# Kernel optimization log

Measured on AMD Instinct MI355X. Metric: run time of the kernel, lower is better.

## Reference

```python
import jax, jax.numpy as jnp
import numpy as np

T, B, I, H = 512, 256, 256, 512  # seq_len, batch, input_size, hidden_size


def setup_inputs() -> dict:
    key = jax.random.key(0)
    ks = jax.random.split(key, 7)
    sc = 1.0 / np.sqrt(H)  # PyTorch nn.RNN init scale ~ U(-1/sqrt(H), 1/sqrt(H)); use scaled normal
    return {
        "x": jax.random.normal(ks[0], (T, B, I), dtype=jnp.float32),
        "w_ih": jax.random.normal(ks[1], (H, I), dtype=jnp.float32) * sc,
        "w_hh": jax.random.normal(ks[2], (H, H), dtype=jnp.float32) * sc,
        "b_ih": jax.random.normal(ks[3], (H,), dtype=jnp.float32) * sc,
        "b_hh": jax.random.normal(ks[4], (H,), dtype=jnp.float32) * sc,
        "w_fc": jax.random.normal(ks[5], (I, H), dtype=jnp.float32) * sc,
        "b_fc": jax.random.normal(ks[6], (I,), dtype=jnp.float32) * sc,
    }


def reference(x, w_ih, w_hh, b_ih, b_hh, w_fc, b_fc):
    # Single-layer tanh RNN (h0 = 0): h_t = tanh(x_t W_ih^T + b_ih + h_{t-1} W_hh^T + b_hh)
    # Hoist the input projection out of the recurrence (one big GEMM).
    xp = jnp.einsum('tbi,hi->tbh', x, w_ih) + b_ih + b_hh  # [T,B,H]
    h0 = jnp.zeros((x.shape[1], w_hh.shape[0]), dtype=x.dtype)

    def step(h, xt):
        h_new = jnp.tanh(xt + h @ w_hh.T)
        return h_new, h_new

    _, hs = jax.lax.scan(step, h0, xp)  # hs: [T,B,H]
    # Output head: Linear(hidden_size -> input_size)
    return jnp.einsum('tbh,oh->tbo', hs, w_fc) + b_fc  # [T,B,I]
```

## Files before the change

### kernel.cpp

```cpp
#include <hip/hip_runtime.h>
#include <hip/hip_bf16.h>

#define T_ 512
#define B_ 256
#define I_ 256
#define H_ 512

#define NG 16
#define NS 4

#define RING_WPG (H_ * 8)
#define RING_BYTES (2ull * NG * RING_WPG * 8)

typedef _Float16 f16x8 __attribute__((ext_vector_type(8)));
typedef float f32x4 __attribute__((ext_vector_type(4)));

__device__ __forceinline__ float tanh_fast(float v) {
  float e = __expf(2.0f * v);
  return 1.0f - 2.0f / (e + 1.0f);
}

__device__ __forceinline__ f16x8 cvt8(const float4 a, const float4 b) {
  f16x8 f;
  f[0] = (_Float16)a.x; f[1] = (_Float16)a.y; f[2] = (_Float16)a.z; f[3] = (_Float16)a.w;
  f[4] = (_Float16)b.x; f[5] = (_Float16)b.y; f[6] = (_Float16)b.z; f[7] = (_Float16)b.w;
  return f;
}

__device__ __forceinline__ unsigned long long pack2h(_Float16 a, _Float16 b, unsigned tag) {
  unsigned ua = __builtin_bit_cast(unsigned short, a);
  unsigned ub = __builtin_bit_cast(unsigned short, b);
  return (unsigned long long)(ua | (ub << 16)) | ((unsigned long long)tag << 32);
}

__global__ __launch_bounds__(256, 1) void rnn_recurrence(
    const float* __restrict__ x,
    const float* __restrict__ w_ih,
    const float* __restrict__ w_hh,
    const float* __restrict__ b_ih,
    const float* __restrict__ b_hh,
    unsigned long long* __restrict__ ring,
    _Float16* __restrict__ hs)
{
  const int tid  = threadIdx.x;
  const int lane = tid & 63;
  const int w    = tid >> 6;
  const int bid  = blockIdx.x;
  const int g    = bid & 15;
  const int s    = bid >> 4;
  const int r0   = g * 16;
  const int c0   = s * 128;
  const int lrow = lane & 15;
  const int quad = lane >> 4;
  const int kq   = quad * 8;

  __shared__ _Float16 hbuf[16][512 + 8];
  __shared__ _Float16 xbuf[16][256 + 8];

  f16x8 whh0[16], whh1[16];
  f16x8 wih0[8], wih1[8];
  const int n0c = c0 + (2 * w + 0) * 16 + lrow;
  const int n1c = c0 + (2 * w + 1) * 16 + lrow;
  const float bias0 = b_ih[n0c] + b_hh[n0c];
  const float bias1 = b_ih[n1c] + b_hh[n1c];
  #pragma unroll
  for (int kt = 0; kt < 16; ++kt) {
    const int k = kt * 32 + kq;
    whh0[kt] = cvt8(*(const float4*)(w_hh + (size_t)n0c * H_ + k),
                    *(const float4*)(w_hh + (size_t)n0c * H_ + k + 4));
    whh1[kt] = cvt8(*(const float4*)(w_hh + (size_t)n1c * H_ + k),
                    *(const float4*)(w_hh + (size_t)n1c * H_ + k + 4));
  }
  #pragma unroll
  for (int kt = 0; kt < 8; ++kt) {
    const int k = kt * 32 + kq;
    wih0[kt] = cvt8(*(const float4*)(w_ih + (size_t)n0c * I_ + k),
                    *(const float4*)(w_ih + (size_t)n0c * I_ + k + 4));
    wih1[kt] = cvt8(*(const float4*)(w_ih + (size_t)n1c * I_ + k),
                    *(const float4*)(w_ih + (size_t)n1c * I_ + k + 4));
  }

  int colf[12], prow[12];
  int roff[12];
  #pragma unroll
  for (int j = 0; j < 12; ++j) {
    const int wdx = tid + j * 256;
    const int rs  = wdx >> 10;
    const int sl  = rs + (rs >= s ? 1 : 0);
    const int c   = (wdx >> 3) & 127;
    const int p   = wdx & 7;
    colf[j] = sl * 128 + c;
    prow[j] = p * 2;
    roff[j] = colf[j] * 8 + p;
  }

  {
    const int row = tid >> 4, ch = tid & 15;
    f16x8 z = {0, 0, 0, 0, 0, 0, 0, 0};
    *(f16x8*)(&hbuf[row][c0 + ch * 8]) = z;
  }

  for (int t = 0; t < T_; ++t) {
    {
      const float* src = x + ((size_t)t * B_ + r0) * I_;
      #pragma unroll
      for (int c = tid; c < 512; c += 256) {
        const int row = c >> 5;
        const int col = (c & 31) * 8;
        *(f16x8*)(&xbuf[row][col]) =
            cvt8(*(const float4*)(src + (size_t)row * I_ + col),
                 *(const float4*)(src + (size_t)row * I_ + col + 4));
      }
    }
    {
      const unsigned long long* rg =
          ring + ((size_t)((t & 1) ? NG : 0) + g) * RING_WPG;
      unsigned long long v[12];
      #pragma unroll
      for (int j = 0; j < 12; ++j)
        v[j] = __hip_atomic_load(&rg[roff[j]], __ATOMIC_RELAXED,
                                 __HIP_MEMORY_SCOPE_AGENT);
      bool again = true;
      while (again) {
        again = false;
        #pragma unroll
        for (int j = 0; j < 12; ++j) {
          if ((unsigned)(v[j] >> 32) != (unsigned)t) {
            v[j] = __hip_atomic_load(&rg[roff[j]], __ATOMIC_RELAXED,
                                     __HIP_MEMORY_SCOPE_AGENT);
            again = true;
          }
        }
      }
      #pragma unroll
      for (int j = 0; j < 12; ++j) {
        const unsigned lo = (unsigned)v[j];
        hbuf[prow[j] + 0][colf[j]] =
            __builtin_bit_cast(_Float16, (unsigned short)(lo & 0xffff));
        hbuf[prow[j] + 1][colf[j]] =
            __builtin_bit_cast(_Float16, (unsigned short)(lo >> 16));
      }
    }
    __syncthreads();

    if (t > 0) {
      const int row = tid >> 4, ch = tid & 15;
      *(uint4*)(hs + ((size_t)(t - 1) * B_ + r0 + row) * H_ + c0 + ch * 8) =
          *(const uint4*)(&hbuf[row][c0 + ch * 8]);
    }

    f32x4 a0a = {0.f,0.f,0.f,0.f}, a0b = {0.f,0.f,0.f,0.f};
    f32x4 a1a = {0.f,0.f,0.f,0.f}, a1b = {0.f,0.f,0.f,0.f};
    #pragma unroll
    for (int kt = 0; kt < 8; ++kt) {
      const f16x8 a = *(const f16x8*)(&hbuf[lrow][kt * 32 + kq]);
      a0a = __builtin_amdgcn_mfma_f32_16x16x32_f16(a, whh0[kt], a0a, 0, 0, 0);
      a1a = __builtin_amdgcn_mfma_f32_16x16x32_f16(a, whh1[kt], a1a, 0, 0, 0);
    }
    #pragma unroll
    for (int kt = 8; kt < 16; ++kt) {
      const f16x8 a = *(const f16x8*)(&hbuf[lrow][kt * 32 + kq]);
      a0b = __builtin_amdgcn_mfma_f32_16x16x32_f16(a, whh0[kt], a0b, 0, 0, 0);
      a1b = __builtin_amdgcn_mfma_f32_16x16x32_f16(a, whh1[kt], a1b, 0, 0, 0);
    }
    #pragma unroll
    for (int kt = 0; kt < 4; ++kt) {
      const f16x8 a = *(const f16x8*)(&xbuf[lrow][kt * 32 + kq]);
      a0a = __builtin_amdgcn_mfma_f32_16x16x32_f16(a, wih0[kt], a0a, 0, 0, 0);
      a1a = __builtin_amdgcn_mfma_f32_16x16x32_f16(a, wih1[kt], a1a, 0, 0, 0);
    }
    #pragma unroll
    for (int kt = 4; kt < 8; ++kt) {
      const f16x8 a = *(const f16x8*)(&xbuf[lrow][kt * 32 + kq]);
      a0b = __builtin_amdgcn_mfma_f32_16x16x32_f16(a, wih0[kt], a0b, 0, 0, 0);
      a1b = __builtin_amdgcn_mfma_f32_16x16x32_f16(a, wih1[kt], a1b, 0, 0, 0);
    }
    const f32x4 acc0 = a0a + a0b;
    const f32x4 acc1 = a1a + a1b;

    __syncthreads();

    _Float16 e0[4], e1[4];
    #pragma unroll
    for (int r = 0; r < 4; ++r) {
      e0[r] = (_Float16)tanh_fast(acc0[r] + bias0);
      e1[r] = (_Float16)tanh_fast(acc1[r] + bias1);
      hbuf[quad * 4 + r][n0c] = e0[r];
      hbuf[quad * 4 + r][n1c] = e1[r];
    }
    {
      unsigned long long* rn =
          ring + ((size_t)(((t + 1) & 1) ? NG : 0) + g) * RING_WPG;
      const unsigned tag = (unsigned)(t + 1);
      __hip_atomic_store(&rn[n0c * 8 + quad * 2 + 0], pack2h(e0[0], e0[1], tag),
                         __ATOMIC_RELAXED, __HIP_MEMORY_SCOPE_AGENT);
      __hip_atomic_store(&rn[n0c * 8 + quad * 2 + 1], pack2h(e0[2], e0[3], tag),
                         __ATOMIC_RELAXED, __HIP_MEMORY_SCOPE_AGENT);
      __hip_atomic_store(&rn[n1c * 8 + quad * 2 + 0], pack2h(e1[0], e1[1], tag),
                         __ATOMIC_RELAXED, __HIP_MEMORY_SCOPE_AGENT);
      __hip_atomic_store(&rn[n1c * 8 + quad * 2 + 1], pack2h(e1[2], e1[3], tag),
                         __ATOMIC_RELAXED, __HIP_MEMORY_SCOPE_AGENT);
    }
  }

  __syncthreads();
  {
    const int row = tid >> 4, ch = tid & 15;
    *(uint4*)(hs + ((size_t)(T_ - 1) * B_ + r0 + row) * H_ + c0 + ch * 8) =
        *(const uint4*)(&hbuf[row][c0 + ch * 8]);
  }
}

__global__ __launch_bounds__(256) void fc_head(
    const _Float16* __restrict__ hs,
    const float* __restrict__ w_fc,
    const float* __restrict__ b_fc,
    float* __restrict__ out)
{
  const int tid  = threadIdx.x;
  const int lane = tid & 63;
  const int w    = tid >> 6;
  const int wm   = w & 1;
  const int wn   = w >> 1;
  const int m0   = blockIdx.x * 64;
  const int n0   = blockIdx.y * 64;
  const int lrow = lane & 15;
  const int quad = lane >> 4;
  const int kq   = quad * 8;

  __shared__ _Float16 As[64][32 + 8];
  __shared__ _Float16 Bs[64][32 + 8];

  f32x4 acc00 = {0.f,0.f,0.f,0.f}, acc01 = {0.f,0.f,0.f,0.f};
  f32x4 acc10 = {0.f,0.f,0.f,0.f}, acc11 = {0.f,0.f,0.f,0.f};

  const int srow = tid >> 2;
  const int skc  = (tid & 3) * 8;

  for (int k0 = 0; k0 < H_; k0 += 32) {
    *(uint4*)(&As[srow][skc]) =
        *(const uint4*)(hs + (size_t)(m0 + srow) * H_ + k0 + skc);
    *(f16x8*)(&Bs[srow][skc]) =
        cvt8(*(const float4*)(w_fc + (size_t)(n0 + srow) * H_ + k0 + skc),
             *(const float4*)(w_fc + (size_t)(n0 + srow) * H_ + k0 + skc + 4));
    __syncthreads();

    const f16x8 a0 = *(const f16x8*)(&As[wm * 32 + lrow][kq]);
    const f16x8 a1 = *(const f16x8*)(&As[wm * 32 + 16 + lrow][kq]);
    const f16x8 b0 = *(const f16x8*)(&Bs[wn * 32 + lrow][kq]);
    const f16x8 b1 = *(const f16x8*)(&Bs[wn * 32 + 16 + lrow][kq]);
    acc00 = __builtin_amdgcn_mfma_f32_16x16x32_f16(a0, b0, acc00, 0, 0, 0);
    acc01 = __builtin_amdgcn_mfma_f32_16x16x32_f16(a0, b1, acc01, 0, 0, 0);
    acc10 = __builtin_amdgcn_mfma_f32_16x16x32_f16(a1, b0, acc10, 0, 0, 0);
    acc11 = __builtin_amdgcn_mfma_f32_16x16x32_f16(a1, b1, acc11, 0, 0, 0);
    __syncthreads();
  }

  #pragma unroll
  for (int ni = 0; ni < 2; ++ni) {
    const int col = n0 + wn * 32 + ni * 16 + lrow;
    const float bf = b_fc[col];
    #pragma unroll
    for (int mi = 0; mi < 2; ++mi) {
      const f32x4 a = (mi == 0) ? (ni == 0 ? acc00 : acc01)
                                : (ni == 0 ? acc10 : acc11);
      #pragma unroll
      for (int r = 0; r < 4; ++r) {
        const int rowm = m0 + wm * 32 + mi * 16 + quad * 4 + r;
        out[(size_t)rowm * I_ + col] = a[r] + bf;
      }
    }
  }
}

extern "C" void kernel_launch(void* const* d_in, const int* in_sizes, int n_in,
                              void* d_out, int out_size, void* d_ws, size_t ws_size,
                              hipStream_t stream) {
  const float* x    = (const float*)d_in[0];
  const float* w_ih = (const float*)d_in[1];
  const float* w_hh = (const float*)d_in[2];
  const float* b_ih = (const float*)d_in[3];
  const float* b_hh = (const float*)d_in[4];
  const float* w_fc = (const float*)d_in[5];
  const float* b_fc = (const float*)d_in[6];
  float* out = (float*)d_out;

  unsigned long long* ring = (unsigned long long*)d_ws;
  _Float16* hs = (_Float16*)((char*)d_ws + RING_BYTES);

  hipMemsetAsync(d_ws, 0, (size_t)NG * RING_WPG * 8, stream);

  rnn_recurrence<<<64, 256, 0, stream>>>(x, w_ih, w_hh, b_ih, b_hh, ring, hs);
  fc_head<<<dim3(2048, 4), 256, 0, stream>>>(hs, w_fc, b_fc, out);
}
```

Baseline: 1.996 ms.

## Overlap local-slice MFMAs and x loads with remote hidden-state polling

```diff
diff --git a/kernel.cpp b/kernel.cpp
--- a/kernel.cpp
+++ b/kernel.cpp
@@ -65,7 +65,8 @@
   const float bias1 = b_ih[n1c] + b_hh[n1c];
   #pragma unroll
   for (int kt = 0; kt < 16; ++kt) {
-    const int k = kt * 32 + kq;
+    const int pk = (s * 4 + kt) & 15;
+    const int k  = pk * 32 + kq;
     whh0[kt] = cvt8(*(const float4*)(w_hh + (size_t)n0c * H_ + k),
                     *(const float4*)(w_hh + (size_t)n0c * H_ + k + 4));
     whh1[kt] = cvt8(*(const float4*)(w_hh + (size_t)n1c * H_ + k),
@@ -80,7 +81,6 @@
                     *(const float4*)(w_ih + (size_t)n1c * I_ + k + 4));
   }
 
-  int colf[12], prow[12];
   int roff[12];
   #pragma unroll
   for (int j = 0; j < 12; ++j) {
@@ -89,9 +89,7 @@
     const int sl  = rs + (rs >= s ? 1 : 0);
     const int c   = (wdx >> 3) & 127;
     const int p   = wdx & 7;
-    colf[j] = sl * 128 + c;
-    prow[j] = p * 2;
-    roff[j] = colf[j] * 8 + p;
+    roff[j] = (sl * 128 + c) * 8 + p;
   }
 
   {
@@ -99,27 +97,46 @@
     f16x8 z = {0, 0, 0, 0, 0, 0, 0, 0};
     *(f16x8*)(&hbuf[row][c0 + ch * 8]) = z;
   }
+  __syncthreads();
+
+  const int xrow = tid >> 5;
+  const int xcol = (tid & 31) * 8;
 
   for (int t = 0; t < T_; ++t) {
+    const unsigned long long* rg =
+        ring + ((size_t)((t & 1) ? NG : 0) + g) * RING_WPG;
+    unsigned long long v[12];
+    #pragma unroll
+    for (int j = 0; j < 12; ++j)
+      v[j] = __hip_atomic_load(&rg[roff[j]], __ATOMIC_RELAXED,
+                               __HIP_MEMORY_SCOPE_AGENT);
+
+    const float* src = x + ((size_t)t * B_ + r0) * I_;
+    const float4 xv0 = *(const float4*)(src + (size_t)xrow * I_ + xcol);
+    const float4 xv1 = *(const float4*)(src + (size_t)xrow * I_ + xcol + 4);
+    const float4 xv2 = *(const float4*)(src + (size_t)(xrow + 8) * I_ + xcol);
+    const float4 xv3 = *(const float4*)(src + (size_t)(xrow + 8) * I_ + xcol + 4);
+
+    if (t > 0) {
+      const int row = tid >> 4, ch = tid & 15;
+      *(uint4*)(hs + ((size_t)(t - 1) * B_ + r0 + row) * H_ + c0 + ch * 8) =
+          *(const uint4*)(&hbuf[row][c0 + ch * 8]);
+    }
+
+    f32x4 a0a = {0.f,0.f,0.f,0.f}, a0b = {0.f,0.f,0.f,0.f};
+    f32x4 a1a = {0.f,0.f,0.f,0.f}, a1b = {0.f,0.f,0.f,0.f};
+    #pragma unroll
+    for (int kt = 0; kt < 4; ++kt) {
+      const int pk = (s * 4 + kt) & 15;
+      const f16x8 a = *(const f16x8*)(&hbuf[lrow][pk * 32 + kq]);
+      a0b = __builtin_amdgcn_mfma_f32_16x16x32_f16(a, whh0[kt], a0b, 0, 0, 0);
+      a1b = __builtin_amdgcn_mfma_f32_16x16x32_f16(a, whh1[kt], a1b, 0, 0, 0);
+    }
+
+    *(f16x8*)(&xbuf[xrow][xcol])     = cvt8(xv0, xv1);
+    *(f16x8*)(&xbuf[xrow + 8][xcol]) = cvt8(xv2, xv3);
+
     {
-      const float* src = x + ((size_t)t * B_ + r0) * I_;
-      #pragma unroll
-      for (int c = tid; c < 512; c += 256) {
-        const int row = c >> 5;
-        const int col = (c & 31) * 8;
-        *(f16x8*)(&xbuf[row][col]) =
-            cvt8(*(const float4*)(src + (size_t)row * I_ + col),
-                 *(const float4*)(src + (size_t)row * I_ + col + 4));
-      }
-    }
-    {
-      const unsigned long long* rg =
-          ring + ((size_t)((t & 1) ? NG : 0) + g) * RING_WPG;
-      unsigned long long v[12];
-      #pragma unroll
-      for (int j = 0; j < 12; ++j)
-        v[j] = __hip_atomic_load(&rg[roff[j]], __ATOMIC_RELAXED,
-                                 __HIP_MEMORY_SCOPE_AGENT);
       bool again = true;
       while (again) {
         again = false;
@@ -134,59 +151,48 @@
       }
       #pragma unroll
       for (int j = 0; j < 12; ++j) {
+        const int col = roff[j] >> 3;
+        const int pr  = (roff[j] & 7) * 2;
         const unsigned lo = (unsigned)v[j];
-        hbuf[prow[j] + 0][colf[j]] =
+        hbuf[pr + 0][col] =
             __builtin_bit_cast(_Float16, (unsigned short)(lo & 0xffff));
-        hbuf[prow[j] + 1][colf[j]] =
+        hbuf[pr + 1][col] =
             __builtin_bit_cast(_Float16, (unsigned short)(lo >> 16));
       }
     }
     __syncthreads();
 
-    if (t > 0) {
-      const int row = tid >> 4, ch = tid & 15;
-      *(uint4*)(hs + ((size_t)(t - 1) * B_ + r0 + row) * H_ + c0 + ch * 8) =
-          *(const uint4*)(&hbuf[row][c0 + ch * 8]);
-    }
-
-    f32x4 a0a = {0.f,0.f,0.f,0.f}, a0b = {0.f,0.f,0.f,0.f};
-    f32x4 a1a = {0.f,0.f,0.f,0.f}, a1b = {0.f,0.f,0.f,0.f};
+    #pragma unroll
+    for (int kt = 4; kt < 16; ++kt) {
+      const int pk = (s * 4 + kt) & 15;
+      const f16x8 a = *(const f16x8*)(&hbuf[lrow][pk * 32 + kq]);
+      if (kt < 10) {
+        a0a = __builtin_amdgcn_mfma_f32_16x16x32_f16(a, whh0[kt], a0a, 0, 0, 0);
+        a1a = __builtin_amdgcn_mfma_f32_16x16x32_f16(a, whh1[kt], a1a, 0, 0, 0);
+      } else {
+        a0b = __builtin_amdgcn_mfma_f32_16x16x32_f16(a, whh0[kt], a0b, 0, 0, 0);
+        a1b = __builtin_amdgcn_mfma_f32_16x16x32_f16(a, whh1[kt], a1b, 0, 0, 0);
+      }
+    }
     #pragma unroll
     for (int kt = 0; kt < 8; ++kt) {
-      const f16x8 a = *(const f16x8*)(&hbuf[lrow][kt * 32 + kq]);
-      a0a = __builtin_amdgcn_mfma_f32_16x16x32_f16(a, whh0[kt], a0a, 0, 0, 0);
-      a1a = __builtin_amdgcn_mfma_f32_16x16x32_f16(a, whh1[kt], a1a, 0, 0, 0);
-    }
-    #pragma unroll
-    for (int kt = 8; kt < 16; ++kt) {
-      const f16x8 a = *(const f16x8*)(&hbuf[lrow][kt * 32 + kq]);
-      a0b = __builtin_amdgcn_mfma_f32_16x16x32_f16(a, whh0[kt], a0b, 0, 0, 0);
-      a1b = __builtin_amdgcn_mfma_f32_16x16x32_f16(a, whh1[kt], a1b, 0, 0, 0);
-    }
-    #pragma unroll
-    for (int kt = 0; kt < 4; ++kt) {
       const f16x8 a = *(const f16x8*)(&xbuf[lrow][kt * 32 + kq]);
-      a0a = __builtin_amdgcn_mfma_f32_16x16x32_f16(a, wih0[kt], a0a, 0, 0, 0);
-      a1a = __builtin_amdgcn_mfma_f32_16x16x32_f16(a, wih1[kt], a1a, 0, 0, 0);
-    }
-    #pragma unroll
-    for (int kt = 4; kt < 8; ++kt) {
-      const f16x8 a = *(const f16x8*)(&xbuf[lrow][kt * 32 + kq]);
-      a0b = __builtin_amdgcn_mfma_f32_16x16x32_f16(a, wih0[kt], a0b, 0, 0, 0);
-      a1b = __builtin_amdgcn_mfma_f32_16x16x32_f16(a, wih1[kt], a1b, 0, 0, 0);
+      if (kt < 4) {
+        a0a = __builtin_amdgcn_mfma_f32_16x16x32_f16(a, wih0[kt], a0a, 0, 0, 0);
+        a1a = __builtin_amdgcn_mfma_f32_16x16x32_f16(a, wih1[kt], a1a, 0, 0, 0);
+      } else {
+        a0b = __builtin_amdgcn_mfma_f32_16x16x32_f16(a, wih0[kt], a0b, 0, 0, 0);
+        a1b = __builtin_amdgcn_mfma_f32_16x16x32_f16(a, wih1[kt], a1b, 0, 0, 0);
+      }
     }
     const f32x4 acc0 = a0a + a0b;
     const f32x4 acc1 = a1a + a1b;
-
-    __syncthreads();
 
     _Float16 e0[4], e1[4];
     #pragma unroll
     for (int r = 0; r < 4; ++r) {
       e0[r] = (_Float16)tanh_fast(acc0[r] + bias0);
       e1[r] = (_Float16)tanh_fast(acc1[r] + bias1);
-      hbuf[quad * 4 + r][n0c] = e0[r];
-      hbuf[quad * 4 + r][n1c] = e1[r];
     }
     {
       unsigned long long* rn =
@@ -201,9 +207,14 @@
       __hip_atomic_store(&rn[n1c * 8 + quad * 2 + 1], pack2h(e1[2], e1[3], tag),
                          __ATOMIC_RELAXED, __HIP_MEMORY_SCOPE_AGENT);
     }
-  }
-
-  __syncthreads();
+    #pragma unroll
+    for (int r = 0; r < 4; ++r) {
+      hbuf[quad * 4 + r][n0c] = e0[r];
+      hbuf[quad * 4 + r][n1c] = e1[r];
+    }
+    __syncthreads();
+  }
+
   {
     const int row = tid >> 4, ch = tid & 15;
     *(uint4*)(hs + ((size_t)(T_ - 1) * B_ + r0 + row) * H_ + c0 + ch * 8) =
@@ -222,8 +233,8 @@
   const int w    = tid >> 6;
   const int wm   = w & 1;
   const int wn   = w >> 1;
-  const int m0   = blockIdx.x * 64;
-  const int n0   = blockIdx.y * 64;
+  const int m0   = blockIdx.y * 64;
+  const int n0   = blockIdx.x * 64;
   const int lrow = lane & 15;
   const int quad = lane >> 4;
   const int kq   = quad * 8;
@@ -291,5 +302,5 @@
   hipMemsetAsync(d_ws, 0, (size_t)NG * RING_WPG * 8, stream);
 
   rnn_recurrence<<<64, 256, 0, stream>>>(x, w_ih, w_hh, b_ih, b_hh, ring, hs);
-  fc_head<<<dim3(2048, 4), 256, 0, stream>>>(hs, w_fc, b_fc, out);
-}
+  fc_head<<<dim3(4, 2048), 256, 0, stream>>>(hs, w_fc, b_fc, out);
+}
```

Result: faster. 1.932 ms (-3.2%).
